# Kernel tuning notes

Hardware: AMD Instinct MI355X
Metric: run time of the kernel (lower is better)

## Reference

```python
import jax, jax.numpy as jnp
import numpy as np

N_NODES = 50000
N_EDGES = 800000
IN_DIM = 50
HIDDEN = 256
N_CLASSES = 121
EPS = 1e-12


def setup_inputs() -> dict:
    key = jax.random.key(0)
    ks = jax.random.split(key, 12)
    p = lambda i, shape: (jax.random.normal(ks[i], shape, dtype=jnp.float32) * 0.05)
    x = jax.random.normal(ks[0], (N_NODES, IN_DIM), dtype=jnp.float32)
    edge_index = jax.random.randint(ks[1], (2, N_EDGES), 0, N_NODES, dtype=jnp.int64)
    return {
        "x": x,
        "edge_index": edge_index,
        # SAGEConv layer 1: lin_l (aggregated, with bias), lin_r (root, no bias)
        "w1_l": p(2, (IN_DIM, HIDDEN)), "b1": p(3, (HIDDEN,)), "w1_r": p(4, (IN_DIM, HIDDEN)),
        # parallel Linear 1
        "wl1": p(5, (IN_DIM, HIDDEN)), "bl1": p(6, (HIDDEN,)),
        # SAGEConv layer 2
        "w2_l": p(7, (HIDDEN, N_CLASSES)), "b2": p(8, (N_CLASSES,)), "w2_r": p(9, (HIDDEN, N_CLASSES)),
        # parallel Linear 2
        "wl2": p(10, (HIDDEN, N_CLASSES)), "bl2": p(11, (N_CLASSES,)),
    }


def _sage_conv(x, src, dst, w_l, b, w_r):
    # mean-aggregate source features at destination nodes (PyG SAGEConv, aggr='mean')
    n = x.shape[0]
    agg = jax.ops.segment_sum(x[src], dst, num_segments=n)            # [N, d]
    deg = jax.ops.segment_sum(jnp.ones((src.shape[0], 1), x.dtype), dst, num_segments=n)
    mean = agg / jnp.maximum(deg, 1.0)
    out = mean @ w_l + b + x @ w_r
    # normalize=True -> L2 row normalization (F.normalize semantics)
    norm = jnp.sqrt(jnp.sum(out * out, axis=-1, keepdims=True))
    return out / jnp.maximum(norm, EPS)


def reference(x, edge_index, w1_l, b1, w1_r, wl1, bl1, w2_l, b2, w2_r, wl2, bl2):
    src, dst = edge_index[0], edge_index[1]
    h = jax.nn.elu(_sage_conv(x, src, dst, w1_l, b1, w1_r) + (x @ wl1 + bl1))
    out = _sage_conv(h, src, dst, w2_l, b2, w2_r) + (h @ wl2 + bl2)
    return out
```

## Files before the change

### kernel.cpp

```cpp
#include <hip/hip_runtime.h>
#include <hip/hip_bf16.h>
#include <math.h>

typedef __hip_bfloat16 bf16;
typedef __attribute__((ext_vector_type(8))) short short8;
typedef __attribute__((ext_vector_type(4))) float f32x4;

#define N_NODES 50000
#define N_EDGES 800000
#define IN_DIM 50
#define HIDDEN 256
#define NCLS 121
#define PSTR 128
#define LDSPITCH 264
#define NCHUNK 196
#define P2ROWS 64

#define OFF_OFF   50048
#define OFF_CSR   150160
#define OFF_HB    950272
#define OFF_PB    7350272
#define OFF_AB    10550272
#define OFF_QRB   15000272
#define OFF_QLB   18200272
#define OFF_BW    21400272
#define OFF_BW1   21449424
#define OFF_CSUM  21482240
#define OFF_CBASE 21482496

__device__ __forceinline__ int clampi(int v, int hi) {
    return v < 0 ? 0 : (v >= hi ? hi - 1 : v);
}

__device__ __forceinline__ float uf(unsigned u) { return __uint_as_float(u); }

__global__ __launch_bounds__(256) void prep_r20(
    const float* __restrict__ x, bf16* __restrict__ xbp, bf16* __restrict__ ab,
    const float* __restrict__ w1l, const float* __restrict__ w1r,
    const float* __restrict__ wl1, bf16* __restrict__ bw1,
    const float* __restrict__ w2l, const float* __restrict__ w2r,
    const float* __restrict__ wl2, bf16* __restrict__ bw,
    int* __restrict__ degi) {
    int b = blockIdx.x;
    if (b < 25000) {
        int i = b * 256 + threadIdx.x;
        int n = i >> 7, c = i & 127;
        float v = 0.0f;
        if (c >= 64 && c < 64 + IN_DIM) v = x[n * IN_DIM + (c - 64)];
        ab[i] = __float2bfloat16(v);
        if (c < 64) {
            float xv = (c < IN_DIM) ? x[n * IN_DIM + c] : 0.0f;
            xbp[n * 64 + c] = __float2bfloat16(xv);
        }
    } else if (b < 25256) {
        int i = (b - 25000) * 256 + threadIdx.x;
        int kt = i / 16384, r = i % 16384, c = r / 32, t32 = r % 32;
        int q = t32 >> 3, j = t32 & 7;
        int k = kt * 32 + q * 8 + j;
        float v = 0.0f;
        if (k < 64) {
            if (k < IN_DIM && c < 256) v = w1l[k * HIDDEN + c];
        } else {
            int kr = k - 64;
            if (kr < IN_DIM)
                v = (c < 256) ? w1r[kr * HIDDEN + c] : wl1[kr * HIDDEN + (c - 256)];
        }
        bw1[i] = __float2bfloat16(v);
    } else if (b < 25640) {
        int i = (b - 25256) * 256 + threadIdx.x;
        int kt = i / 12288, r = i % 12288, c = r / 32, t32 = r % 32;
        int q = t32 >> 3, j = t32 & 7;
        int k = kt * 32 + q * 8 + j;
        int mat = c >> 7, cls = c & 127;
        float v = 0.0f;
        if (cls < NCLS) {
            const float* w = (mat == 0) ? w2l : ((mat == 1) ? w2r : wl2);
            v = w[k * NCLS + cls];
        }
        bw[i] = __float2bfloat16(v);
    } else {
        int i = (b - 25640) * 256 + threadIdx.x;
        if (i < N_NODES) degi[i] = 0;
    }
}

__global__ __launch_bounds__(256) void degrank_r20(const int* __restrict__ dst,
                                                   int* __restrict__ degi,
                                                   int* __restrict__ rank) {
    int e = blockIdx.x * 256 + threadIdx.x;
    if (e < N_EDGES) {
        int d = clampi(dst[e], N_NODES);
        rank[e] = atomicAdd(&degi[d], 1);
    }
}

__global__ __launch_bounds__(256) void chunksum_r20(const int* __restrict__ degi,
                                                    int* __restrict__ csum) {
    __shared__ int red[256];
    int i = blockIdx.x * 256 + threadIdx.x;
    red[threadIdx.x] = (i < N_NODES) ? degi[i] : 0;
    __syncthreads();
    for (int s = 128; s > 0; s >>= 1) {
        if (threadIdx.x < s) red[threadIdx.x] += red[threadIdx.x + s];
        __syncthreads();
    }
    if (threadIdx.x == 0) csum[blockIdx.x] = red[0];
}

__global__ __launch_bounds__(256) void scanchunks_r20(const int* __restrict__ csum,
                                                      int* __restrict__ cbase,
                                                      int* __restrict__ off) {
    __shared__ int s[256];
    int t = threadIdx.x;
    int v = (t < NCHUNK) ? csum[t] : 0;
    s[t] = v;
    __syncthreads();
    for (int d = 1; d < 256; d <<= 1) {
        int u = (t >= d) ? s[t - d] : 0;
        __syncthreads();
        s[t] += u;
        __syncthreads();
    }
    if (t < NCHUNK) cbase[t] = s[t] - v;
    if (t == 255) off[N_NODES] = s[255];
}

__global__ __launch_bounds__(256) void scatteroff_r20(const int* __restrict__ degi,
                                                      const int* __restrict__ cbase,
                                                      int* __restrict__ off) {
    __shared__ int s[256];
    int i = blockIdx.x * 256 + threadIdx.x;
    int t = threadIdx.x;
    int v = (i < N_NODES) ? degi[i] : 0;
    s[t] = v;
    __syncthreads();
    for (int d = 1; d < 256; d <<= 1) {
        int u = (t >= d) ? s[t - d] : 0;
        __syncthreads();
        s[t] += u;
        __syncthreads();
    }
    int ex = s[t] - v + cbase[blockIdx.x];
    if (i < N_NODES) off[i] = ex;
}

__global__ __launch_bounds__(256) void csrfill2_r20(const int* __restrict__ src,
                                                    const int* __restrict__ dst,
                                                    const int* __restrict__ rank,
                                                    const int* __restrict__ off,
                                                    int* __restrict__ csr) {
    int e = blockIdx.x * 256 + threadIdx.x;
    if (e >= N_EDGES) return;
    int d = clampi(dst[e], N_NODES);
    csr[off[d] + rank[e]] = clampi(src[e], N_NODES);
}

__global__ __launch_bounds__(256) void gather1_r20(
    const uint2* __restrict__ xb2, const int* __restrict__ off,
    const int* __restrict__ csr, const int* __restrict__ degi,
    unsigned int* __restrict__ abu) {
    __shared__ float rdeg[8];
    int base = blockIdx.x * 8;
    int tid = threadIdx.x;
    if (tid < 8) rdeg[tid] = 1.0f / fmaxf((float)degi[base + tid], 1.0f);
    __syncthreads();
    int wave = tid >> 6, lane = tid & 63;
    int half = lane >> 5;
    int grp = (lane >> 4) & 1;
    int lg = lane & 15;
    int n = wave * 2 + half;
    int node = base + n;
    int e0 = off[node], e1 = off[node + 1];
    float a0 = 0, a1 = 0, a2 = 0, a3 = 0;
    float b0 = 0, b1 = 0, b2 = 0, b3 = 0;
    int e = e0;
    for (; e + 4 <= e1; e += 4) {
        int r0 = csr[e + grp];
        int r1 = csr[e + 2 + grp];
        uint2 u0 = xb2[(size_t)r0 * 16 + lg];
        uint2 u1 = xb2[(size_t)r1 * 16 + lg];
        a0 += uf(u0.x << 16);
        a1 += uf(u0.x & 0xffff0000u);
        a2 += uf(u0.y << 16);
        a3 += uf(u0.y & 0xffff0000u);
        b0 += uf(u1.x << 16);
        b1 += uf(u1.x & 0xffff0000u);
        b2 += uf(u1.y << 16);
        b3 += uf(u1.y & 0xffff0000u);
    }
    for (; e < e1; e += 2) {
        int idx = e + grp;
        int safe = idx < e1 ? idx : e;
        int r0 = csr[safe];
        uint2 u0 = xb2[(size_t)r0 * 16 + lg];
        if (idx < e1) {
            a0 += uf(u0.x << 16);
            a1 += uf(u0.x & 0xffff0000u);
            a2 += uf(u0.y << 16);
            a3 += uf(u0.y & 0xffff0000u);
        }
    }
    a0 += b0;
    a1 += b1;
    a2 += b2;
    a3 += b3;
    a0 += __shfl_xor(a0, 16, 64);
    a1 += __shfl_xor(a1, 16, 64);
    a2 += __shfl_xor(a2, 16, 64);
    a3 += __shfl_xor(a3, 16, 64);
    if (grp == 0) {
        float r = rdeg[n];
        bf16 v0 = __float2bfloat16(a0 * r), v1 = __float2bfloat16(a1 * r);
        bf16 v2 = __float2bfloat16(a2 * r), v3 = __float2bfloat16(a3 * r);
        unsigned p0 = (unsigned)*(unsigned short*)&v0 |
                      ((unsigned)*(unsigned short*)&v1 << 16);
        unsigned p1 = (unsigned)*(unsigned short*)&v2 |
                      ((unsigned)*(unsigned short*)&v3 << 16);
        abu[(size_t)node * 64 + 2 * lg] = p0;
        abu[(size_t)node * 64 + 2 * lg + 1] = p1;
    }
}

__global__ __launch_bounds__(256) void proj1_r20(
    const bf16* __restrict__ ab_, const bf16* __restrict__ bw1,
    const float* __restrict__ b1, const float* __restrict__ bl1,
    bf16* __restrict__ hb) {
    __shared__ float os[16][516];
    __shared__ float partial[16][17];
    __shared__ float rns[16];

    int base = blockIdx.x * 16;
    int tid = threadIdx.x;
    int wave = tid >> 6, lane = tid & 63;
    int rc = lane & 15, quad = lane >> 4;

    const short* ab = (const short*)ab_;
    short8 af[4];
#pragma unroll
    for (int kt = 0; kt < 4; ++kt)
        af[kt] = *(const short8*)&ab[(size_t)(base + rc) * 128 + kt * 32 + quad * 8];

    const short* bws = (const short*)bw1;
    for (int ti = 0; ti < 8; ++ti) {
        int t = wave * 8 + ti;
        f32x4 acc = {0.0f, 0.0f, 0.0f, 0.0f};
#pragma unroll
        for (int kt = 0; kt < 4; ++kt) {
            short8 bf = *(const short8*)
                &bws[(((size_t)kt * 512 + t * 16 + rc) * 4 + quad) * 8];
            acc = __builtin_amdgcn_mfma_f32_16x16x32_bf16(af[kt], bf, acc, 0, 0, 0);
        }
        int col = t * 16 + rc;
#pragma unroll
        for (int r = 0; r < 4; ++r) os[quad * 4 + r][col] = acc[r];
    }
    __syncthreads();
    {
        int n = tid & 15, jj = tid >> 4;
        float s = 0.0f;
#pragma unroll
        for (int c = 0; c < 16; ++c) {
            int cc = jj * 16 + c;
            float v = os[n][cc] + b1[cc];
            s += v * v;
        }
        partial[n][jj] = s;
    }
    __syncthreads();
    if (tid < 16) {
        float s = 0.0f;
#pragma unroll
        for (int jj = 0; jj < 16; ++jj) s += partial[tid][jj];
        rns[tid] = 1.0f / fmaxf(sqrtf(s), 1e-12f);
    }
    __syncthreads();
    for (int i = 0; i < 16; ++i) {
        int idx = i * 256 + tid;
        int n = idx >> 8, c = idx & 255;
        float z = (os[n][c] + b1[c]) * rns[n] + os[n][256 + c] + bl1[c];
        hb[(size_t)(base + n) * HIDDEN + c] =
            __float2bfloat16(z > 0.0f ? z : expm1f(z));
    }
}

__global__ __launch_bounds__(256) void proj2_r20(
    const bf16* __restrict__ hb, const bf16* __restrict__ bw,
    bf16* __restrict__ pb, bf16* __restrict__ qrb, bf16* __restrict__ qlb) {
    __shared__ __align__(16) short hs[P2ROWS * LDSPITCH];

    int base = blockIdx.x * P2ROWS;
    int tid = threadIdx.x;
    const short* hbs = (const short*)hb;
#pragma unroll
    for (int i = 0; i < 8; ++i) {
        int f = tid + 256 * i;
        int row = f >> 5, u4 = f & 31;
        *(uint4*)&hs[row * LDSPITCH + u4 * 8] =
            *(const uint4*)(hbs + (size_t)(base + row) * HIDDEN + u4 * 8);
    }
    __syncthreads();

    int wave = tid >> 6, lane = tid & 63;
    int rc = lane & 15, quad = lane >> 4;

    short8 af[4][8];
#pragma unroll
    for (int rg = 0; rg < 4; ++rg)
#pragma unroll
        for (int kt = 0; kt < 8; ++kt)
            af[rg][kt] = *(const short8*)
                &hs[(rg * 16 + rc) * LDSPITCH + kt * 32 + quad * 8];

    const short* bws = (const short*)bw;
    for (int ti = 0; ti < 6; ++ti) {
        int t = wave * 6 + ti;
        f32x4 acc[4] = {{0, 0, 0, 0}, {0, 0, 0, 0}, {0, 0, 0, 0}, {0, 0, 0, 0}};
#pragma unroll
        for (int kt = 0; kt < 8; ++kt) {
            short8 bf = *(const short8*)
                &bws[(((size_t)kt * 384 + t * 16 + rc) * 4 + quad) * 8];
#pragma unroll
            for (int rg = 0; rg < 4; ++rg)
                acc[rg] = __builtin_amdgcn_mfma_f32_16x16x32_bf16(af[rg][kt], bf,
                                                                  acc[rg], 0, 0, 0);
        }
        int col = t * 16 + rc;
        int mat = col >> 7, cls = col & 127;
        bf16* dstp = (mat == 0) ? pb : ((mat == 1) ? qrb : qlb);
#pragma unroll
        for (int rg = 0; rg < 4; ++rg)
#pragma unroll
            for (int r = 0; r < 4; ++r) {
                int node = base + rg * 16 + quad * 4 + r;
                if (node < N_NODES)
                    dstp[(size_t)node * PSTR + cls] = __float2bfloat16(acc[rg][r]);
            }
    }
}

__global__ __launch_bounds__(256) void final_r20(
    const bf16* __restrict__ pb, const bf16* __restrict__ qrb,
    const bf16* __restrict__ qlb, const int* __restrict__ off,
    const int* __restrict__ csr, const int* __restrict__ degi,
    const float* __restrict__ b2, const float* __restrict__ bl2,
    float* __restrict__ out) {
    __shared__ float mp[8][128];
    __shared__ float red[8][128];
    __shared__ float rdeg[8];

    const uint4* pbu4 = (const uint4*)pb;
    int base = blockIdx.x * 8;
    int tid = threadIdx.x;
    if (tid < 8) rdeg[tid] = 1.0f / fmaxf((float)degi[base + tid], 1.0f);
    int wv = tid >> 6, lane = tid & 63;
    int g = lane >> 4, lg = lane & 15;
#pragma unroll
    for (int i = 0; i < 2; ++i) {
        int n = wv * 2 + i;
        int node = base + n;
        int e0 = off[node], e1 = off[node + 1];
        float a[8] = {0, 0, 0, 0, 0, 0, 0, 0};
        float b[8] = {0, 0, 0, 0, 0, 0, 0, 0};
        int e = e0;
        for (; e + 8 <= e1; e += 8) {
            int r0 = csr[e + g];
            int r1 = csr[e + 4 + g];
            uint4 u0 = pbu4[(size_t)r0 * 16 + lg];
            uint4 u1 = pbu4[(size_t)r1 * 16 + lg];
            a[0] += uf(u0.x << 16);
            a[1] += uf(u0.x & 0xffff0000u);
            a[2] += uf(u0.y << 16);
            a[3] += uf(u0.y & 0xffff0000u);
            a[4] += uf(u0.z << 16);
            a[5] += uf(u0.z & 0xffff0000u);
            a[6] += uf(u0.w << 16);
            a[7] += uf(u0.w & 0xffff0000u);
            b[0] += uf(u1.x << 16);
            b[1] += uf(u1.x & 0xffff0000u);
            b[2] += uf(u1.y << 16);
            b[3] += uf(u1.y & 0xffff0000u);
            b[4] += uf(u1.z << 16);
            b[5] += uf(u1.z & 0xffff0000u);
            b[6] += uf(u1.w << 16);
            b[7] += uf(u1.w & 0xffff0000u);
        }
        for (; e < e1; e += 4) {
            int idx = e + g;
            int safe = idx < e1 ? idx : e;
            int r0 = csr[safe];
            uint4 u0 = pbu4[(size_t)r0 * 16 + lg];
            if (idx < e1) {
                a[0] += uf(u0.x << 16);
                a[1] += uf(u0.x & 0xffff0000u);
                a[2] += uf(u0.y << 16);
                a[3] += uf(u0.y & 0xffff0000u);
                a[4] += uf(u0.z << 16);
                a[5] += uf(u0.z & 0xffff0000u);
                a[6] += uf(u0.w << 16);
                a[7] += uf(u0.w & 0xffff0000u);
            }
        }
#pragma unroll
        for (int k = 0; k < 8; ++k) a[k] += b[k];
#pragma unroll
        for (int k = 0; k < 8; ++k) {
            a[k] += __shfl_xor(a[k], 16, 64);
            a[k] += __shfl_xor(a[k], 32, 64);
        }
        if (g == 0) {
#pragma unroll
            for (int k = 0; k < 8; ++k) mp[n][8 * lg + k] = a[k];
        }
    }
    __syncthreads();

    int j = tid & 127, gg = tid >> 7;
    float bj = (j < NCLS) ? b2[j] : 0.0f;
    float blj = (j < NCLS) ? bl2[j] : 0.0f;
    float out2[4];
#pragma unroll
    for (int i = 0; i < 4; ++i) {
        int n = gg * 4 + i;
        out2[i] = (j < NCLS)
                      ? (mp[n][j] * rdeg[n] + bj +
                         __bfloat162float(qrb[(size_t)(base + n) * PSTR + j]))
                      : 0.0f;
        red[n][j] = out2[i] * out2[i];
    }
    __syncthreads();
    for (int stride = 64; stride > 0; stride >>= 1) {
        if (j < stride) {
#pragma unroll
            for (int i = 0; i < 4; ++i)
                red[gg * 4 + i][j] += red[gg * 4 + i][j + stride];
        }
        __syncthreads();
    }
    if (j < NCLS) {
#pragma unroll
        for (int i = 0; i < 4; ++i) {
            int n = gg * 4 + i;
            float rn = 1.0f / fmaxf(sqrtf(red[n][0]), 1e-12f);
            out[(base + n) * NCLS + j] =
                out2[i] * rn +
                __bfloat162float(qlb[(size_t)(base + n) * PSTR + j]) + blj;
        }
    }
}

extern "C" void kernel_launch(void* const* d_in, const int* in_sizes, int n_in,
                              void* d_out, int out_size, void* d_ws, size_t ws_size,
                              hipStream_t stream) {
    const float* x   = (const float*)d_in[0];
    const int*   ei  = (const int*)d_in[1];
    const float* w1l = (const float*)d_in[2];
    const float* b1  = (const float*)d_in[3];
    const float* w1r = (const float*)d_in[4];
    const float* wl1 = (const float*)d_in[5];
    const float* bl1 = (const float*)d_in[6];
    const float* w2l = (const float*)d_in[7];
    const float* b2  = (const float*)d_in[8];
    const float* w2r = (const float*)d_in[9];
    const float* wl2 = (const float*)d_in[10];
    const float* bl2 = (const float*)d_in[11];
    float* out = (float*)d_out;

    const int* src = ei;
    const int* dst = ei + N_EDGES;

    int*   wsI   = (int*)d_ws;
    float* wsF   = (float*)d_ws;
    int*   degi  = wsI;
    int*   off   = wsI + OFF_OFF;
    int*   csr   = wsI + OFF_CSR;
    bf16*  hb    = (bf16*)(wsF + OFF_HB);
    int*   rank  = (int*)(wsF + OFF_HB);
    bf16*  pb    = (bf16*)(wsF + OFF_PB);
    bf16*  xbp   = (bf16*)(wsF + OFF_PB);
    bf16*  ab    = (bf16*)(wsF + OFF_AB);
    bf16*  qrb   = (bf16*)(wsF + OFF_QRB);
    bf16*  qlb   = (bf16*)(wsF + OFF_QLB);
    bf16*  bw    = (bf16*)(wsF + OFF_BW);
    bf16*  bw1   = (bf16*)(wsF + OFF_BW1);
    int*   csum  = wsI + OFF_CSUM;
    int*   cbase = wsI + OFF_CBASE;

    prep_r20<<<25836, 256, 0, stream>>>(x, xbp, ab, w1l, w1r, wl1, bw1,
                                        w2l, w2r, wl2, bw, degi);

    degrank_r20<<<(N_EDGES + 255) / 256, 256, 0, stream>>>(dst, degi, rank);

    chunksum_r20<<<NCHUNK, 256, 0, stream>>>(degi, csum);
    scanchunks_r20<<<1, 256, 0, stream>>>(csum, cbase, off);
    scatteroff_r20<<<NCHUNK, 256, 0, stream>>>(degi, cbase, off);

    csrfill2_r20<<<(N_EDGES + 255) / 256, 256, 0, stream>>>(src, dst, rank, off, csr);

    gather1_r20<<<N_NODES / 8, 256, 0, stream>>>((const uint2*)xbp, off,
                                                 csr, degi, (unsigned int*)ab);
    proj1_r20<<<N_NODES / 16, 256, 0, stream>>>(ab, bw1, b1, bl1, hb);
    proj2_r20<<<(N_NODES + P2ROWS - 1) / P2ROWS, 256, 0, stream>>>(hb, bw, pb, qrb, qlb);
    final_r20<<<N_NODES / 8, 256, 0, stream>>>(pb, qrb, qlb,
                                               off, csr, degi, b2, bl2, out);
}
```

Measured before the change: 287.0 us.

## Fuse scan kernels, stage CSR indices in LDS, widen proj1 tile

Merges the single-block chunk scan and the offset scatter into one kernel. Each block redundantly rescans the chunk sums, which saves a launch and a global round-trip. The gather1 and final kernels now preload the block's node offsets and, when they fit, up to 1024 neighbour indices into shared memory, so the inner loops avoid dependent global index loads. proj1 now handles 32 rows per block, reusing each weight fragment across two MFMAs, and keeps the parallel-linear half in bf16 in LDS to save shared-memory space. The costs are extra LDS use, which may lower occupancy, plus added branching, and the parallel-linear result is now rounded to bf16.

```diff
diff --git a/kernel.cpp b/kernel.cpp
--- a/kernel.cpp
+++ b/kernel.cpp
@@ -15,6 +15,9 @@
 #define LDSPITCH 264
 #define NCHUNK 196
 #define P2ROWS 64
+#define P1ROWS 32
+#define P1PITCH 261
+#define FEDGE 1024
 
 #define OFF_OFF   50048
 #define OFF_CSR   150160
@@ -26,7 +29,6 @@
 #define OFF_BW    21400272
 #define OFF_BW1   21449424
 #define OFF_CSUM  21482240
-#define OFF_CBASE 21482496
 
 __device__ __forceinline__ int clampi(int v, int hi) {
     return v < 0 ? 0 : (v >= hi ? hi - 1 : v);
@@ -34,7 +36,7 @@
 
 __device__ __forceinline__ float uf(unsigned u) { return __uint_as_float(u); }
 
-__global__ __launch_bounds__(256) void prep_r20(
+__global__ __launch_bounds__(256) void prep_r21(
     const float* __restrict__ x, bf16* __restrict__ xbp, bf16* __restrict__ ab,
     const float* __restrict__ w1l, const float* __restrict__ w1r,
     const float* __restrict__ wl1, bf16* __restrict__ bw1,
@@ -84,7 +86,7 @@
     }
 }
 
-__global__ __launch_bounds__(256) void degrank_r20(const int* __restrict__ dst,
+__global__ __launch_bounds__(256) void degrank_r21(const int* __restrict__ dst,
                                                    int* __restrict__ degi,
                                                    int* __restrict__ rank) {
     int e = blockIdx.x * 256 + threadIdx.x;
@@ -94,7 +96,7 @@
     }
 }
 
-__global__ __launch_bounds__(256) void chunksum_r20(const int* __restrict__ degi,
+__global__ __launch_bounds__(256) void chunksum_r21(const int* __restrict__ degi,
                                                     int* __restrict__ csum) {
     __shared__ int red[256];
     int i = blockIdx.x * 256 + threadIdx.x;
@@ -107,13 +109,26 @@
     if (threadIdx.x == 0) csum[blockIdx.x] = red[0];
 }
 
-__global__ __launch_bounds__(256) void scanchunks_r20(const int* __restrict__ csum,
-                                                      int* __restrict__ cbase,
-                                                      int* __restrict__ off) {
+__global__ __launch_bounds__(256) void scanscatter_r21(const int* __restrict__ csum,
+                                                       const int* __restrict__ degi,
+                                                       int* __restrict__ off) {
+    __shared__ int cs[256];
     __shared__ int s[256];
     int t = threadIdx.x;
-    int v = (t < NCHUNK) ? csum[t] : 0;
-    s[t] = v;
+    int cv = (t < NCHUNK) ? csum[t] : 0;
+    cs[t] = cv;
+    __syncthreads();
+    for (int d = 1; d < 256; d <<= 1) {
+        int u = (t >= d) ? cs[t - d] : 0;
+        __syncthreads();
+        cs[t] += u;
+        __syncthreads();
+    }
+    int cb = cs[blockIdx.x] - csum[blockIdx.x];
+    if (blockIdx.x == 0 && t == 0) off[N_NODES] = cs[NCHUNK - 1];
+    int i = blockIdx.x * 256 + t;
+    int dv = (i < N_NODES) ? degi[i] : 0;
+    s[t] = dv;
     __syncthreads();
     for (int d = 1; d < 256; d <<= 1) {
         int u = (t >= d) ? s[t - d] : 0;
@@ -121,30 +136,10 @@
         s[t] += u;
         __syncthreads();
     }
-    if (t < NCHUNK) cbase[t] = s[t] - v;
-    if (t == 255) off[N_NODES] = s[255];
-}
-
-__global__ __launch_bounds__(256) void scatteroff_r20(const int* __restrict__ degi,
-                                                      const int* __restrict__ cbase,
-                                                      int* __restrict__ off) {
-    __shared__ int s[256];
-    int i = blockIdx.x * 256 + threadIdx.x;
-    int t = threadIdx.x;
-    int v = (i < N_NODES) ? degi[i] : 0;
-    s[t] = v;
-    __syncthreads();
-    for (int d = 1; d < 256; d <<= 1) {
-        int u = (t >= d) ? s[t - d] : 0;
-        __syncthreads();
-        s[t] += u;
-        __syncthreads();
-    }
-    int ex = s[t] - v + cbase[blockIdx.x];
-    if (i < N_NODES) off[i] = ex;
-}
-
-__global__ __launch_bounds__(256) void csrfill2_r20(const int* __restrict__ src,
+    if (i < N_NODES) off[i] = s[t] - dv + cb;
+}
+
+__global__ __launch_bounds__(256) void csrfill2_r21(const int* __restrict__ src,
                                                     const int* __restrict__ dst,
                                                     const int* __restrict__ rank,
                                                     const int* __restrict__ off,
@@ -155,28 +150,38 @@
     csr[off[d] + rank[e]] = clampi(src[e], N_NODES);
 }
 
-__global__ __launch_bounds__(256) void gather1_r20(
+__global__ __launch_bounds__(256) void gather1_r21(
     const uint2* __restrict__ xb2, const int* __restrict__ off,
     const int* __restrict__ csr, const int* __restrict__ degi,
     unsigned int* __restrict__ abu) {
     __shared__ float rdeg[8];
+    __shared__ int soff[9];
+    __shared__ int sidx[FEDGE];
     int base = blockIdx.x * 8;
     int tid = threadIdx.x;
+    if (tid < 9) soff[tid] = off[base + tid];
     if (tid < 8) rdeg[tid] = 1.0f / fmaxf((float)degi[base + tid], 1.0f);
     __syncthreads();
+    int e0b = soff[0];
+    int count = soff[8] - e0b;
+    bool inl = (count <= FEDGE);
+    if (inl)
+        for (int i = tid; i < count; i += 256) sidx[i] = csr[e0b + i];
+    __syncthreads();
+
     int wave = tid >> 6, lane = tid & 63;
     int half = lane >> 5;
     int grp = (lane >> 4) & 1;
     int lg = lane & 15;
     int n = wave * 2 + half;
     int node = base + n;
-    int e0 = off[node], e1 = off[node + 1];
+    int e0 = soff[n], e1 = soff[n + 1];
     float a0 = 0, a1 = 0, a2 = 0, a3 = 0;
     float b0 = 0, b1 = 0, b2 = 0, b3 = 0;
     int e = e0;
     for (; e + 4 <= e1; e += 4) {
-        int r0 = csr[e + grp];
-        int r1 = csr[e + 2 + grp];
+        int r0 = inl ? sidx[e + grp - e0b] : csr[e + grp];
+        int r1 = inl ? sidx[e + 2 + grp - e0b] : csr[e + 2 + grp];
         uint2 u0 = xb2[(size_t)r0 * 16 + lg];
         uint2 u1 = xb2[(size_t)r1 * 16 + lg];
         a0 += uf(u0.x << 16);
@@ -191,7 +196,7 @@
     for (; e < e1; e += 2) {
         int idx = e + grp;
         int safe = idx < e1 ? idx : e;
-        int r0 = csr[safe];
+        int r0 = inl ? sidx[safe - e0b] : csr[safe];
         uint2 u0 = xb2[(size_t)r0 * 16 + lg];
         if (idx < e1) {
             a0 += uf(u0.x << 16);
@@ -221,69 +226,94 @@
     }
 }
 
-__global__ __launch_bounds__(256) void proj1_r20(
+__global__ __launch_bounds__(256) void proj1_r21(
     const bf16* __restrict__ ab_, const bf16* __restrict__ bw1,
     const float* __restrict__ b1, const float* __restrict__ bl1,
     bf16* __restrict__ hb) {
-    __shared__ float os[16][516];
-    __shared__ float partial[16][17];
-    __shared__ float rns[16];
-
-    int base = blockIdx.x * 16;
+    __shared__ float osA[P1ROWS][P1PITCH];
+    __shared__ short osB[P1ROWS][256];
+    __shared__ float partial[P1ROWS][9];
+    __shared__ float rns[P1ROWS];
+
+    int base = blockIdx.x * P1ROWS;
     int tid = threadIdx.x;
     int wave = tid >> 6, lane = tid & 63;
     int rc = lane & 15, quad = lane >> 4;
 
     const short* ab = (const short*)ab_;
-    short8 af[4];
-#pragma unroll
-    for (int kt = 0; kt < 4; ++kt)
-        af[kt] = *(const short8*)&ab[(size_t)(base + rc) * 128 + kt * 32 + quad * 8];
+    short8 af[2][4];
+#pragma unroll
+    for (int rg = 0; rg < 2; ++rg)
+#pragma unroll
+        for (int kt = 0; kt < 4; ++kt)
+            af[rg][kt] = *(const short8*)
+                &ab[(size_t)(base + rg * 16 + rc) * 128 + kt * 32 + quad * 8];
 
     const short* bws = (const short*)bw1;
     for (int ti = 0; ti < 8; ++ti) {
         int t = wave * 8 + ti;
-        f32x4 acc = {0.0f, 0.0f, 0.0f, 0.0f};
+        f32x4 acc[2] = {{0, 0, 0, 0}, {0, 0, 0, 0}};
 #pragma unroll
         for (int kt = 0; kt < 4; ++kt) {
             short8 bf = *(const short8*)
                 &bws[(((size_t)kt * 512 + t * 16 + rc) * 4 + quad) * 8];
-            acc = __builtin_amdgcn_mfma_f32_16x16x32_bf16(af[kt], bf, acc, 0, 0, 0);
+#pragma unroll
+            for (int rg = 0; rg < 2; ++rg)
+                acc[rg] = __builtin_amdgcn_mfma_f32_16x16x32_bf16(af[rg][kt], bf,
+                                                                  acc[rg], 0, 0, 0);
         }
         int col = t * 16 + rc;
-#pragma unroll
-        for (int r = 0; r < 4; ++r) os[quad * 4 + r][col] = acc[r];
+        if (col < 256) {
+#pragma unroll
+            for (int rg = 0; rg < 2; ++rg)
+#pragma unroll
+                for (int r = 0; r < 4; ++r)
+                    osA[rg * 16 + quad * 4 + r][col] = acc[rg][r];
+        } else {
+#pragma unroll
+            for (int rg = 0; rg < 2; ++rg)
+#pragma unroll
+                for (int r = 0; r < 4; ++r) {
+                    bf16 v = __float2bfloat16(acc[rg][r]);
+                    osB[rg * 16 + quad * 4 + r][col - 256] = *(short*)&v;
+                }
+        }
     }
     __syncthreads();
     {
-        int n = tid & 15, jj = tid >> 4;
+        int n = tid & 31, jj = tid >> 5;
         float s = 0.0f;
 #pragma unroll
-        for (int c = 0; c < 16; ++c) {
-            int cc = jj * 16 + c;
-            float v = os[n][cc] + b1[cc];
+        for (int c = 0; c < 32; ++c) {
+            int cc = jj * 32 + c;
+            float v = osA[n][cc] + b1[cc];
             s += v * v;
         }
         partial[n][jj] = s;
     }
     __syncthreads();
-    if (tid < 16) {
+    if (tid < 32) {
         float s = 0.0f;
 #pragma unroll
-        for (int jj = 0; jj < 16; ++jj) s += partial[tid][jj];
+        for (int jj = 0; jj < 8; ++jj) s += partial[tid][jj];
         rns[tid] = 1.0f / fmaxf(sqrtf(s), 1e-12f);
     }
     __syncthreads();
-    for (int i = 0; i < 16; ++i) {
+    for (int i = 0; i < 32; ++i) {
         int idx = i * 256 + tid;
         int n = idx >> 8, c = idx & 255;
-        float z = (os[n][c] + b1[c]) * rns[n] + os[n][256 + c] + bl1[c];
-        hb[(size_t)(base + n) * HIDDEN + c] =
-            __float2bfloat16(z > 0.0f ? z : expm1f(z));
-    }
-}
-
-__global__ __launch_bounds__(256) void proj2_r20(
+        int node = base + n;
+        if (node < N_NODES) {
+            short sb = osB[n][c];
+            float lin = __bfloat162float(*(bf16*)&sb);
+            float z = (osA[n][c] + b1[c]) * rns[n] + lin + bl1[c];
+            hb[(size_t)node * HIDDEN + c] =
+                __float2bfloat16(z > 0.0f ? z : expm1f(z));
+        }
+    }
+}
+
+__global__ __launch_bounds__(256) void proj2_r21(
     const bf16* __restrict__ hb, const bf16* __restrict__ bw,
     bf16* __restrict__ pb, bf16* __restrict__ qrb, bf16* __restrict__ qlb) {
     __shared__ __align__(16) short hs[P2ROWS * LDSPITCH];
@@ -338,7 +368,7 @@
     }
 }
 
-__global__ __launch_bounds__(256) void final_r20(
+__global__ __launch_bounds__(256) void final_r21(
     const bf16* __restrict__ pb, const bf16* __restrict__ qrb,
     const bf16* __restrict__ qlb, const int* __restrict__ off,
     const int* __restrict__ csr, const int* __restrict__ degi,
@@ -347,24 +377,34 @@
     __shared__ float mp[8][128];
     __shared__ float red[8][128];
     __shared__ float rdeg[8];
+    __shared__ int soff[9];
+    __shared__ int sidx[FEDGE];
 
     const uint4* pbu4 = (const uint4*)pb;
     int base = blockIdx.x * 8;
     int tid = threadIdx.x;
+    if (tid < 9) soff[tid] = off[base + tid];
     if (tid < 8) rdeg[tid] = 1.0f / fmaxf((float)degi[base + tid], 1.0f);
+    __syncthreads();
+    int e0b = soff[0];
+    int count = soff[8] - e0b;
+    bool inl = (count <= FEDGE);
+    if (inl)
+        for (int i = tid; i < count; i += 256) sidx[i] = csr[e0b + i];
+    __syncthreads();
+
     int wv = tid >> 6, lane = tid & 63;
     int g = lane >> 4, lg = lane & 15;
 #pragma unroll
     for (int i = 0; i < 2; ++i) {
         int n = wv * 2 + i;
-        int node = base + n;
-        int e0 = off[node], e1 = off[node + 1];
+        int e0 = soff[n], e1 = soff[n + 1];
         float a[8] = {0, 0, 0, 0, 0, 0, 0, 0};
         float b[8] = {0, 0, 0, 0, 0, 0, 0, 0};
         int e = e0;
         for (; e + 8 <= e1; e += 8) {
-            int r0 = csr[e + g];
-            int r1 = csr[e + 4 + g];
+            int r0 = inl ? sidx[e + g - e0b] : csr[e + g];
+            int r1 = inl ? sidx[e + 4 + g - e0b] : csr[e + 4 + g];
             uint4 u0 = pbu4[(size_t)r0 * 16 + lg];
             uint4 u1 = pbu4[(size_t)r1 * 16 + lg];
             a[0] += uf(u0.x << 16);
@@ -387,7 +427,7 @@
         for (; e < e1; e += 4) {
             int idx = e + g;
             int safe = idx < e1 ? idx : e;
-            int r0 = csr[safe];
+            int r0 = inl ? sidx[safe - e0b] : csr[safe];
             uint4 u0 = pbu4[(size_t)r0 * 16 + lg];
             if (idx < e1) {
                 a[0] += uf(u0.x << 16);
@@ -483,23 +523,21 @@
     bf16*  bw    = (bf16*)(wsF + OFF_BW);
     bf16*  bw1   = (bf16*)(wsF + OFF_BW1);
     int*   csum  = wsI + OFF_CSUM;
-    int*   cbase = wsI + OFF_CBASE;
-
-    prep_r20<<<25836, 256, 0, stream>>>(x, xbp, ab, w1l, w1r, wl1, bw1,
+
+    prep_r21<<<25836, 256, 0, stream>>>(x, xbp, ab, w1l, w1r, wl1, bw1,
                                         w2l, w2r, wl2, bw, degi);
 
-    degrank_r20<<<(N_EDGES + 255) / 256, 256, 0, stream>>>(dst, degi, rank);
-
-    chunksum_r20<<<NCHUNK, 256, 0, stream>>>(degi, csum);
-    scanchunks_r20<<<1, 256, 0, stream>>>(csum, cbase, off);
-    scatteroff_r20<<<NCHUNK, 256, 0, stream>>>(degi, cbase, off);
-
-    csrfill2_r20<<<(N_EDGES + 255) / 256, 256, 0, stream>>>(src, dst, rank, off, csr);
-
-    gather1_r20<<<N_NODES / 8, 256, 0, stream>>>((const uint2*)xbp, off,
+    degrank_r21<<<(N_EDGES + 255) / 256, 256, 0, stream>>>(dst, degi, rank);
+
+    chunksum_r21<<<NCHUNK, 256, 0, stream>>>(degi, csum);
+    scanscatter_r21<<<NCHUNK, 256, 0, stream>>>(csum, degi, off);
+
+    csrfill2_r21<<<(N_EDGES + 255) / 256, 256, 0, stream>>>(src, dst, rank, off, csr);
+
+    gather1_r21<<<N_NODES / 8, 256, 0, stream>>>((const uint2*)xbp, off,
                                                  csr, degi, (unsigned int*)ab);
-    proj1_r20<<<N_NODES / 16, 256, 0, stream>>>(ab, bw1, b1, bl1, hb);
-    proj2_r20<<<(N_NODES + P2ROWS - 1) / P2ROWS, 256, 0, stream>>>(hb, bw, pb, qrb, qlb);
-    final_r20<<<N_NODES / 8, 256, 0, stream>>>(pb, qrb, qlb,
+    proj1_r21<<<(N_NODES + P1ROWS - 1) / P1ROWS, 256, 0, stream>>>(ab, bw1, b1, bl1, hb);
+    proj2_r21<<<(N_NODES + P2ROWS - 1) / P2ROWS, 256, 0, stream>>>(hb, bw, pb, qrb, qlb);
+    final_r21<<<N_NODES / 8, 256, 0, stream>>>(pb, qrb, qlb,
                                                off, csr, degi, b2, bl2, out);
 }
```

After: 290.6 us. Within noise of the previous version (+1.3%).
